# Kernel optimization log

Hardware: AMD Instinct MI355X
Metric: run time of the kernel (lower is better)

Reference implementation:

```python
import jax, jax.numpy as jnp
import numpy as np

EPS = 1e-8  # torch.nn.CosineSimilarity default eps


def setup_inputs() -> dict:
    key = jax.random.key(0)
    k1, k2, k3 = jax.random.split(key, 3)
    B, D, C = 262144, 256, 64
    inputs = jax.random.normal(k1, (B, D), dtype=jnp.float32)
    labels = jax.random.randint(k2, (B,), 0, C, dtype=jnp.int64)
    class_avgs = jax.random.normal(k3, (C, D), dtype=jnp.float32)
    return {"inputs": inputs, "labels": labels, "class_avgs": class_avgs}


def reference(inputs, labels, class_avgs):
    # Cosine similarity of every input row against every class centroid.
    # Faithful to the original double loop: classes whose avg vector contains
    # inf get similarity 1.0 (the "unseen class" sentinel branch).
    inf_mask = jnp.any(jnp.isinf(class_avgs), axis=-1)  # (C,)
    x_norm = jnp.linalg.norm(inputs, axis=-1)           # (B,)
    c_norm = jnp.linalg.norm(class_avgs, axis=-1)       # (C,)
    dots = jnp.einsum("bd,cd->bc", inputs, class_avgs)  # (B, C)
    denom = jnp.maximum(x_norm[:, None] * c_norm[None, :], EPS)
    sims = dots / denom
    return jnp.where(inf_mask[None, :], jnp.float32(1.0), sims)
```

## Files before the change

kernel.cpp:

```cpp
#include <hip/hip_runtime.h>
#include <hip/hip_bf16.h>
#include <math.h>


typedef __attribute__((ext_vector_type(8))) short bf16x8;
typedef __attribute__((ext_vector_type(4))) float f32x4;

#define EPS 1e-8f

__device__ __forceinline__ short f2bf(float f) {
  union { float f; unsigned u; } v; v.f = f;
  unsigned r = v.u + 0x7fffu + ((v.u >> 16) & 1u);
  return (short)(r >> 16);
}
__device__ __forceinline__ float bf2f(short s) {
  union { float f; unsigned u; } v;
  v.u = ((unsigned)(unsigned short)s) << 16;
  return v.f;
}

__device__ __forceinline__ void dma16(const float* g, float* l) {
  __builtin_amdgcn_global_load_lds(
      (const __attribute__((address_space(1))) void*)g,
      (__attribute__((address_space(3))) void*)l, 16, 0, 0);
}


__global__ __launch_bounds__(256) void simrel_kernel(
    const float* __restrict__ X,
    const float* __restrict__ CLS,
    float* __restrict__ OUT)
{
  __shared__ __align__(16) float Abuf[4 * 2048];
  __shared__ __align__(16) short Bfrag[8 * 4 * 64 * 8];

  const int tid  = threadIdx.x;
  const int wave = tid >> 6;
  const int lane = tid & 63;
  const int m    = lane & 15;
  const int quad = lane >> 4;

  {
    const int c  = tid >> 2;
    const int qq = tid & 3;
    const float4* src = (const float4*)CLS + c * 64 + qq * 16;
#pragma unroll
    for (int i = 0; i < 16; ++i) {
      float4 v = src[i];
      const int wabs = qq * 64 + i * 4;
      const int ks = wabs >> 5;
      const int w0 = wabs & 31;
      const int h  = w0 >> 4;
      const int qd = (w0 >> 2) & 3;
      const int lb = (qd << 4) | (c & 15);
      const int nt = c >> 4;
      *(short4*)&Bfrag[((ks * 4 + nt) * 64 + lb) * 8 + h * 4] =
          make_short4(f2bf(v.x), f2bf(v.y), f2bf(v.z), f2bf(v.w));
    }
  }
  __syncthreads();

  const size_t rowbase = (size_t)blockIdx.x * 128 + (size_t)wave * 32;

  const float* gbase[2][2];
#pragma unroll
  for (int mti = 0; mti < 2; ++mti)
#pragma unroll
    for (int h = 0; h < 2; ++h)
      gbase[mti][h] = X + (rowbase + mti * 16 + m) * 256 + h * 16 + quad * 4;

  float* abase = &Abuf[wave * 2048];

#pragma unroll
  for (int mti = 0; mti < 2; ++mti)
#pragma unroll
    for (int h = 0; h < 2; ++h)
      dma16(gbase[mti][h], abase + (mti * 2 + h) * 256);

  float cnv[4]; int cflag[4];
#pragma unroll
  for (int nt = 0; nt < 4; ++nt) {
    float s = 0.f;
#pragma unroll
    for (int ks = 0; ks < 8; ++ks) {
      bf16x8 b = *(const bf16x8*)&Bfrag[((ks * 4 + nt) * 64 + lane) * 8];
#pragma unroll
      for (int j = 0; j < 8; ++j) { float f = bf2f(b[j]); s += f * f; }
    }
    s += __shfl_xor(s, 16);
    s += __shfl_xor(s, 32);
    cflag[nt] = !isfinite(s);
    cnv[nt]   = sqrtf(s);
  }

  f32x4 acc[2][4];
#pragma unroll
  for (int mti = 0; mti < 2; ++mti)
#pragma unroll
    for (int nt = 0; nt < 4; ++nt)
      acc[mti][nt] = (f32x4){0.f, 0.f, 0.f, 0.f};
  float ssqr[2] = {0.f, 0.f};

#pragma unroll
  for (int ks = 0; ks < 8; ++ks) {
    if (ks < 7) {
      const int nb = (ks + 1) & 1;
#pragma unroll
      for (int mti = 0; mti < 2; ++mti)
#pragma unroll
        for (int h = 0; h < 2; ++h)
          dma16(gbase[mti][h] + (ks + 1) * 32, abase + (nb * 4 + mti * 2 + h) * 256);
      asm volatile("s_waitcnt vmcnt(4)" ::: "memory");
    } else {
      asm volatile("s_waitcnt vmcnt(0)" ::: "memory");
    }
    const int cb = ks & 1;

    bf16x8 bw[4];
#pragma unroll
    for (int nt = 0; nt < 4; ++nt)
      bw[nt] = *(const bf16x8*)&Bfrag[((ks * 4 + nt) * 64 + lane) * 8];

#pragma unroll
    for (int mti = 0; mti < 2; ++mti) {
      float4 a0 = *(const float4*)(abase + (cb * 4 + mti * 2 + 0) * 256 + lane * 4);
      float4 a1 = *(const float4*)(abase + (cb * 4 + mti * 2 + 1) * 256 + lane * 4);
      ssqr[mti] += a0.x * a0.x + a0.y * a0.y + a0.z * a0.z + a0.w * a0.w +
                   a1.x * a1.x + a1.y * a1.y + a1.z * a1.z + a1.w * a1.w;
      bf16x8 af;
      af[0] = f2bf(a0.x); af[1] = f2bf(a0.y); af[2] = f2bf(a0.z); af[3] = f2bf(a0.w);
      af[4] = f2bf(a1.x); af[5] = f2bf(a1.y); af[6] = f2bf(a1.z); af[7] = f2bf(a1.w);
#pragma unroll
      for (int nt = 0; nt < 4; ++nt)
        acc[mti][nt] =
            __builtin_amdgcn_mfma_f32_16x16x32_bf16(af, bw[nt], acc[mti][nt], 0, 0, 0);
    }
  }

#pragma unroll
  for (int mti = 0; mti < 2; ++mti) {
    float s = ssqr[mti];
    s += __shfl_xor(s, 16);
    s += __shfl_xor(s, 32);
    float xn = sqrtf(s);
    float xnr[4];
#pragma unroll
    for (int r = 0; r < 4; ++r)
      xnr[r] = __shfl(xn, quad * 4 + r);
#pragma unroll
    for (int nt = 0; nt < 4; ++nt) {
      const int n = nt * 16 + m;
#pragma unroll
      for (int r = 0; r < 4; ++r) {
        const size_t row = rowbase + mti * 16 + quad * 4 + r;
        const float d = fmaxf(xnr[r] * cnv[nt], EPS);
        const float v =
            cflag[nt] ? 1.0f : acc[mti][nt][r] * __builtin_amdgcn_rcpf(d);
        OUT[row * 64 + n] = v;
      }
    }
  }
}

extern "C" void kernel_launch(void* const* d_in, const int* in_sizes, int n_in,
                              void* d_out, int out_size, void* d_ws, size_t ws_size,
                              hipStream_t stream) {
  (void)n_in; (void)d_ws; (void)ws_size; (void)out_size;
  const float* X   = (const float*)d_in[0];
  const float* CLS = (const float*)d_in[2];
  float* OUT = (float*)d_out;

  const int Brows  = in_sizes[0] / 256;
  const int blocks = Brows / 128;
  simrel_kernel<<<blocks, 256, 0, stream>>>(X, CLS, OUT);
}
```

Baseline: 387.7 us.

## Load A tiles directly into registers with two-deep prefetch instead of LDS DMA

Drops the global_load_lds staging buffer for the input rows and instead loads each lane's float4 fragments straight into registers, with a register-level pipeline that prefetches two k-steps ahead. This removes the 32KB per-block LDS buffer and the LDS reads. It also adds an occupancy hint through launch_bounds(256,3). In exchange it raises VGPR pressure and relies on the compiler placing vmcnt waits well.

```diff
diff --git a/kernel.cpp b/kernel.cpp
--- a/kernel.cpp
+++ b/kernel.cpp
@@ -1,5 +1,4 @@
 #include <hip/hip_runtime.h>
-#include <hip/hip_bf16.h>
 #include <math.h>
 
 
@@ -19,19 +18,12 @@
   return v.f;
 }
 
-__device__ __forceinline__ void dma16(const float* g, float* l) {
-  __builtin_amdgcn_global_load_lds(
-      (const __attribute__((address_space(1))) void*)g,
-      (__attribute__((address_space(3))) void*)l, 16, 0, 0);
-}
 
-
-__global__ __launch_bounds__(256) void simrel_kernel(
+__global__ __launch_bounds__(256, 3) void simrel_kernel(
     const float* __restrict__ X,
     const float* __restrict__ CLS,
     float* __restrict__ OUT)
 {
-  __shared__ __align__(16) float Abuf[4 * 2048];
   __shared__ __align__(16) short Bfrag[8 * 4 * 64 * 8];
 
   const int tid  = threadIdx.x;
@@ -69,13 +61,14 @@
     for (int h = 0; h < 2; ++h)
       gbase[mti][h] = X + (rowbase + mti * 16 + m) * 256 + h * 16 + quad * 4;
 
-  float* abase = &Abuf[wave * 2048];
-
+  float4 Acur[2][2], Anxt[2][2];
 #pragma unroll
   for (int mti = 0; mti < 2; ++mti)
 #pragma unroll
-    for (int h = 0; h < 2; ++h)
-      dma16(gbase[mti][h], abase + (mti * 2 + h) * 256);
+    for (int h = 0; h < 2; ++h) {
+      Acur[mti][h] = *(const float4*)(gbase[mti][h]);
+      Anxt[mti][h] = *(const float4*)(gbase[mti][h] + 32);
+    }
 
   float cnv[4]; int cflag[4];
 #pragma unroll
@@ -103,18 +96,14 @@
 
 #pragma unroll
   for (int ks = 0; ks < 8; ++ks) {
-    if (ks < 7) {
-      const int nb = (ks + 1) & 1;
+    float4 Apre[2][2];
+    if (ks < 6) {
 #pragma unroll
       for (int mti = 0; mti < 2; ++mti)
 #pragma unroll
         for (int h = 0; h < 2; ++h)
-          dma16(gbase[mti][h] + (ks + 1) * 32, abase + (nb * 4 + mti * 2 + h) * 256);
-      asm volatile("s_waitcnt vmcnt(4)" ::: "memory");
-    } else {
-      asm volatile("s_waitcnt vmcnt(0)" ::: "memory");
+          Apre[mti][h] = *(const float4*)(gbase[mti][h] + (ks + 2) * 32);
     }
-    const int cb = ks & 1;
 
     bf16x8 bw[4];
 #pragma unroll
@@ -123,8 +112,8 @@
 
 #pragma unroll
     for (int mti = 0; mti < 2; ++mti) {
-      float4 a0 = *(const float4*)(abase + (cb * 4 + mti * 2 + 0) * 256 + lane * 4);
-      float4 a1 = *(const float4*)(abase + (cb * 4 + mti * 2 + 1) * 256 + lane * 4);
+      float4 a0 = Acur[mti][0];
+      float4 a1 = Acur[mti][1];
       ssqr[mti] += a0.x * a0.x + a0.y * a0.y + a0.z * a0.z + a0.w * a0.w +
                    a1.x * a1.x + a1.y * a1.y + a1.z * a1.z + a1.w * a1.w;
       bf16x8 af;
@@ -135,6 +124,14 @@
         acc[mti][nt] =
             __builtin_amdgcn_mfma_f32_16x16x32_bf16(af, bw[nt], acc[mti][nt], 0, 0, 0);
     }
+
+#pragma unroll
+    for (int mti = 0; mti < 2; ++mti)
+#pragma unroll
+      for (int h = 0; h < 2; ++h) {
+        Acur[mti][h] = Anxt[mti][h];
+        if (ks < 6) Anxt[mti][h] = Apre[mti][h];
+      }
   }
 
 #pragma unroll
```

Result: slower. 426.1 us (+9.9%).

## Precompute class fragments and norms in a prep kernel; vectorize output stores

Applied to the files above, without the earlier changes.

Adds a small prep kernel that converts the class centroids to bf16 MFMA fragment layout once and computes the class norms and inf flags into workspace. Each main block then DMAs the prepacked fragments into LDS instead of converting them itself and recomputing norms. The MFMA operands are swapped so the accumulator is transposed, which lets each lane write four contiguous output floats as one 16-byte store. The cost is a second launch and a dependency on the workspace buffer.

```diff
diff --git a/kernel.cpp b/kernel.cpp
--- a/kernel.cpp
+++ b/kernel.cpp
@@ -1,5 +1,4 @@
 #include <hip/hip_runtime.h>
-#include <hip/hip_bf16.h>
 #include <math.h>
 
 
@@ -13,22 +12,48 @@
   unsigned r = v.u + 0x7fffu + ((v.u >> 16) & 1u);
   return (short)(r >> 16);
 }
-__device__ __forceinline__ float bf2f(short s) {
-  union { float f; unsigned u; } v;
-  v.u = ((unsigned)(unsigned short)s) << 16;
-  return v.f;
-}
 
-__device__ __forceinline__ void dma16(const float* g, float* l) {
+__device__ __forceinline__ void dma16(const void* g, void* l) {
   __builtin_amdgcn_global_load_lds(
       (const __attribute__((address_space(1))) void*)g,
       (__attribute__((address_space(3))) void*)l, 16, 0, 0);
 }
 
+__global__ __launch_bounds__(256) void simrel_prep(
+    const float* __restrict__ CLS, short* __restrict__ Bws,
+    float* __restrict__ CNws)
+{
+  const int t   = threadIdx.x;
+  const int c   = blockIdx.x * 16 + (t >> 4);
+  const int s16 = t & 15;
+  const float4* src = (const float4*)(CLS + c * 256 + s16 * 16);
+  float s = 0.f, fl = 0.f;
+#pragma unroll
+  for (int i = 0; i < 4; ++i) {
+    float4 v = src[i];
+    s += v.x * v.x + v.y * v.y + v.z * v.z + v.w * v.w;
+    if (isinf(v.x) || isinf(v.y) || isinf(v.z) || isinf(v.w)) fl = 1.f;
+    const int wabs = s16 * 16 + i * 4;
+    const int ks = wabs >> 5;
+    const int w0 = wabs & 31;
+    const int h  = w0 >> 4;
+    const int qd = (w0 >> 2) & 3;
+    const int lb = (qd << 4) | (c & 15);
+    const int nt = c >> 4;
+    *(short4*)&Bws[((ks * 4 + nt) * 64 + lb) * 8 + h * 4] =
+        make_short4(f2bf(v.x), f2bf(v.y), f2bf(v.z), f2bf(v.w));
+  }
+  s  += __shfl_xor(s, 1);  s  += __shfl_xor(s, 2);
+  s  += __shfl_xor(s, 4);  s  += __shfl_xor(s, 8);
+  fl += __shfl_xor(fl, 1); fl += __shfl_xor(fl, 2);
+  fl += __shfl_xor(fl, 4); fl += __shfl_xor(fl, 8);
+  if (s16 == 0) CNws[c] = (fl > 0.f) ? -1.0f : sqrtf(s);
+}
 
 __global__ __launch_bounds__(256) void simrel_kernel(
     const float* __restrict__ X,
-    const float* __restrict__ CLS,
+    const short* __restrict__ Bws,
+    const float* __restrict__ CNws,
     float* __restrict__ OUT)
 {
   __shared__ __align__(16) float Abuf[4 * 2048];
@@ -39,26 +64,6 @@
   const int lane = tid & 63;
   const int m    = lane & 15;
   const int quad = lane >> 4;
-
-  {
-    const int c  = tid >> 2;
-    const int qq = tid & 3;
-    const float4* src = (const float4*)CLS + c * 64 + qq * 16;
-#pragma unroll
-    for (int i = 0; i < 16; ++i) {
-      float4 v = src[i];
-      const int wabs = qq * 64 + i * 4;
-      const int ks = wabs >> 5;
-      const int w0 = wabs & 31;
-      const int h  = w0 >> 4;
-      const int qd = (w0 >> 2) & 3;
-      const int lb = (qd << 4) | (c & 15);
-      const int nt = c >> 4;
-      *(short4*)&Bfrag[((ks * 4 + nt) * 64 + lb) * 8 + h * 4] =
-          make_short4(f2bf(v.x), f2bf(v.y), f2bf(v.z), f2bf(v.w));
-    }
-  }
-  __syncthreads();
 
   const size_t rowbase = (size_t)blockIdx.x * 128 + (size_t)wave * 32;
 
@@ -77,21 +82,22 @@
     for (int h = 0; h < 2; ++h)
       dma16(gbase[mti][h], abase + (mti * 2 + h) * 256);
 
-  float cnv[4]; int cflag[4];
+  {
+    const char* bs = (const char*)Bws;
+    char* bd = (char*)Bfrag;
 #pragma unroll
-  for (int nt = 0; nt < 4; ++nt) {
-    float s = 0.f;
+    for (int i = 0; i < 8; ++i) {
+      const int off = (wave * 8 + i) * 1024;
+      dma16(bs + off + lane * 16, bd + off);
+    }
+  }
+
+  f32x4 cnq[4];
 #pragma unroll
-    for (int ks = 0; ks < 8; ++ks) {
-      bf16x8 b = *(const bf16x8*)&Bfrag[((ks * 4 + nt) * 64 + lane) * 8];
-#pragma unroll
-      for (int j = 0; j < 8; ++j) { float f = bf2f(b[j]); s += f * f; }
-    }
-    s += __shfl_xor(s, 16);
-    s += __shfl_xor(s, 32);
-    cflag[nt] = !isfinite(s);
-    cnv[nt]   = sqrtf(s);
-  }
+  for (int nt = 0; nt < 4; ++nt)
+    cnq[nt] = *(const f32x4*)(CNws + nt * 16 + quad * 4);
+
+  __syncthreads();
 
   f32x4 acc[2][4];
 #pragma unroll
@@ -133,7 +139,7 @@
 #pragma unroll
       for (int nt = 0; nt < 4; ++nt)
         acc[mti][nt] =
-            __builtin_amdgcn_mfma_f32_16x16x32_bf16(af, bw[nt], acc[mti][nt], 0, 0, 0);
+            __builtin_amdgcn_mfma_f32_16x16x32_bf16(bw[nt], af, acc[mti][nt], 0, 0, 0);
     }
   }
 
@@ -142,22 +148,19 @@
     float s = ssqr[mti];
     s += __shfl_xor(s, 16);
     s += __shfl_xor(s, 32);
-    float xn = sqrtf(s);
-    float xnr[4];
-#pragma unroll
-    for (int r = 0; r < 4; ++r)
-      xnr[r] = __shfl(xn, quad * 4 + r);
+    const float xn = sqrtf(s);
+    const size_t row = rowbase + mti * 16 + m;
 #pragma unroll
     for (int nt = 0; nt < 4; ++nt) {
-      const int n = nt * 16 + m;
+      f32x4 o;
 #pragma unroll
       for (int r = 0; r < 4; ++r) {
-        const size_t row = rowbase + mti * 16 + quad * 4 + r;
-        const float d = fmaxf(xnr[r] * cnv[nt], EPS);
-        const float v =
-            cflag[nt] ? 1.0f : acc[mti][nt][r] * __builtin_amdgcn_rcpf(d);
-        OUT[row * 64 + n] = v;
+        const float cn = cnq[nt][r];
+        const float d = fmaxf(xn * cn, EPS);
+        const float v = acc[mti][nt][r] * __builtin_amdgcn_rcpf(d);
+        o[r] = (cn < 0.f) ? 1.0f : v;
       }
+      *(f32x4*)&OUT[row * 64 + nt * 16 + quad * 4] = o;
     }
   }
 }
@@ -165,12 +168,17 @@
 extern "C" void kernel_launch(void* const* d_in, const int* in_sizes, int n_in,
                               void* d_out, int out_size, void* d_ws, size_t ws_size,
                               hipStream_t stream) {
-  (void)n_in; (void)d_ws; (void)ws_size; (void)out_size;
+  (void)n_in; (void)ws_size; (void)out_size;
   const float* X   = (const float*)d_in[0];
   const float* CLS = (const float*)d_in[2];
   float* OUT = (float*)d_out;
 
+  short* Bws  = (short*)d_ws;
+  float* CNws = (float*)((char*)d_ws + 32768);
+
   const int Brows  = in_sizes[0] / 256;
   const int blocks = Brows / 128;
-  simrel_kernel<<<blocks, 256, 0, stream>>>(X, CLS, OUT);
+
+  simrel_prep<<<4, 256, 0, stream>>>(CLS, Bws, CNws);
+  simrel_kernel<<<blocks, 256, 0, stream>>>(X, Bws, CNws, OUT);
 }
```

Result: no change. 382.1 us (-1.5%).
